# Kernel tuning notes

Hardware: AMD Instinct MI355X
Metric: run time of the kernel (lower is better)

## Reference

```python
import jax, jax.numpy as jnp
import numpy as np

V, D, H, S = 100000, 300, 300, 4096   # vocab, embed dim, biLSTM hidden (2x150), seq len
HU = H // 2                            # per-direction LSTM units
NSYN = 4


def _lstm(x, W, U, b):
    """Keras-style LSTM scan. x: [S, D] -> hidden states [S, HU]. Gate order i,f,g,o."""
    def step(carry, xt):
        h, c = carry
        z = xt @ W + h @ U + b              # [4*HU]
        i, f, g, o = jnp.split(z, 4)
        i = jax.nn.sigmoid(i)
        f = jax.nn.sigmoid(f)
        g = jnp.tanh(g)
        o = jax.nn.sigmoid(o)
        c = f * c + i * g
        h = o * jnp.tanh(c)
        return (h, c), h
    init = (jnp.zeros((HU,), x.dtype), jnp.zeros((HU,), x.dtype))
    _, hs = jax.lax.scan(step, init, x)
    return hs


def setup_inputs() -> dict:
    key = jax.random.key(0)
    ks = jax.random.split(key, 20)
    s = 0.05  # small init scale keeps exp() attention scores well-conditioned
    return {
        "sentence": jax.random.randint(ks[0], (S,), 0, V),
        "synonym_indices": jax.random.randint(ks[1], (S, NSYN), 0, V),
        "embedding_matrix": jax.random.normal(ks[2], (V, D), jnp.float32) * s,
        # forward-direction LSTM
        "W_f": jax.random.normal(ks[3], (D, 4 * HU), jnp.float32) * s,
        "U_f": jax.random.normal(ks[4], (HU, 4 * HU), jnp.float32) * s,
        "b_f": jnp.zeros((4 * HU,), jnp.float32),
        # backward-direction LSTM
        "W_b": jax.random.normal(ks[5], (D, 4 * HU), jnp.float32) * s,
        "U_b": jax.random.normal(ks[6], (HU, 4 * HU), jnp.float32) * s,
        "b_b": jnp.zeros((4 * HU,), jnp.float32),
        # primary attention dense (h1 -> h1)
        "W_p": jax.random.normal(ks[7], (H, H), jnp.float32) * s,
        "b_p": jnp.zeros((H,), jnp.float32),
        # secondary attention dense (2*h1 -> 1, tanh)
        "W_s": jax.random.normal(ks[8], (2 * H, 1), jnp.float32) * s,
        "b_s": jnp.zeros((1,), jnp.float32),
        # output heads
        "W_emo": jax.random.normal(ks[9], (2 * H, 8), jnp.float32) * s,
        "b_emo": jnp.zeros((8,), jnp.float32),
        "W_sent": jax.random.normal(ks[10], (2 * H, 1), jnp.float32) * s,
        "b_sent": jnp.zeros((1,), jnp.float32),
    }


def reference(sentence, synonym_indices, embedding_matrix,
              W_f, U_f, b_f, W_b, U_b, b_b,
              W_p, b_p, W_s, b_s, W_emo, b_emo, W_sent, b_sent):
    emb = embedding_matrix[sentence]                       # [S, D] gather
    # bidirectional LSTM (concat fwd and reversed-bwd hidden states)
    h_fwd = _lstm(emb, W_f, U_f, b_f)                      # [S, HU]
    h_bwd = _lstm(emb[::-1], W_b, U_b, b_b)[::-1]          # [S, HU]
    hidden_states = jnp.concatenate([h_fwd, h_bwd], -1)    # [S, H]
    # primary attention: per-word synonym gather + exp-scored weighted sum (vectorized)
    out = hidden_states @ W_p + b_p                        # [S, H]
    syn = embedding_matrix[synonym_indices]                # [S, NSYN, D] irregular gather
    scores = jnp.exp(jnp.einsum('sd,skd->sk', out, syn))   # [S, NSYN]
    m = jnp.einsum('sk,skd->sd', scores, syn)              # [S, D]
    h_hats = jnp.concatenate([hidden_states, m], -1)       # [S, 2H]
    # secondary attention
    coeff = jnp.exp(jnp.tanh(h_hats @ W_s + b_s))          # [S, 1]
    H_HAT = jnp.sum(coeff * h_hats, axis=0)[None, :]       # [1, 2H]
    emotion_logits = H_HAT @ W_emo + b_emo                 # [1, 8]
    sentiment_logits = H_HAT @ W_sent + b_sent             # [1, 1]
    return (emotion_logits, sentiment_logits)
```

## Files before the change

kernel.cpp:

```cpp
#include <hip/hip_runtime.h>
#include <hip/hip_bf16.h>
#include <math.h>

#define S_LEN 4096
#define D_EMB 300
#define NG    600
#define HDIM  300
#define H2    600
#define VOCAB 100000

typedef float v4f __attribute__((ext_vector_type(4)));
typedef _Float16 f16x2 __attribute__((ext_vector_type(2)));
typedef _Float16 f16x8 __attribute__((ext_vector_type(8)));

__device__ __forceinline__ float bf2f(unsigned short u) {
  union { unsigned int i; float f; } v; v.i = ((unsigned int)u) << 16; return v.f;
}
__device__ __forceinline__ unsigned short f2bf(float f) {
  union { float f; unsigned int i; } v; v.f = f;
  return (unsigned short)((v.i + 0x7FFFu + ((v.i >> 16) & 1u)) >> 16);
}

__device__ __forceinline__ void bar_lds() {
  asm volatile("s_waitcnt lgkmcnt(0)\n\ts_barrier" ::: "memory");
}

__global__ void zero_hh(float* __restrict__ HH) {
  if (threadIdx.x < 640) HH[threadIdx.x] = 0.f;
}
__global__ void zero_out_f(float* __restrict__ o, int n) {
  if ((int)threadIdx.x < n) o[threadIdx.x] = 0.f;
}

#define BM 64
#define BN 64
#define BK 16
template<bool A_BF16>
__global__ __launch_bounds__(256) void gemm_bias(
    const void* __restrict__ Av,
    const int* __restrict__ idx, int lda, int nrowsA,
    const float* __restrict__ B,
    const float* __restrict__ bias,
    unsigned short* __restrict__ C,
    int N, int K)
{
  __shared__ __align__(16) float As[BK][BM + 4];
  __shared__ __align__(16) float Bs[BK][BN + 4];
  __shared__ int rowidx[BM];

  int tid = threadIdx.x;
  int bm0 = blockIdx.y * BM, bn0 = blockIdx.x * BN;
  if (tid < BM) {
    int r = idx ? idx[bm0 + tid] : (bm0 + tid);
    r = (r < 0) ? 0 : ((r >= nrowsA) ? (nrowsA - 1) : r);
    rowidx[tid] = r;
  }
  __syncthreads();

  int tx  = tid & 15, ty = tid >> 4;
  int ar  = tid >> 2, akv = (tid & 3) << 2;
  int bkr = tid >> 4, bnv = (tid & 15) << 2;

  float acc[4][4] = {};
  for (int kk = 0; kk < K; kk += BK) {
    float a0=0.f, a1=0.f, a2=0.f, a3=0.f;
    int ka = kk + akv;
    if (ka < K) {
      if (A_BF16) {
        const unsigned short* A = (const unsigned short*)Av;
        ushort4 qa = *(const ushort4*)(A + (size_t)rowidx[ar]*lda + ka);
        a0 = bf2f(qa.x); a1 = bf2f(qa.y); a2 = bf2f(qa.z); a3 = bf2f(qa.w);
      } else {
        const float* A = (const float*)Av;
        float4 qa = *(const float4*)(A + (size_t)rowidx[ar]*lda + ka);
        a0 = qa.x; a1 = qa.y; a2 = qa.z; a3 = qa.w;
      }
    }
    float b0=0.f, b1=0.f, b2=0.f, b3=0.f;
    int kb = kk + bkr, nb = bn0 + bnv;
    if (kb < K && nb < N) {
      float4 qb = *(const float4*)(B + (size_t)kb*N + nb);
      b0 = qb.x; b1 = qb.y; b2 = qb.z; b3 = qb.w;
    }
    As[akv+0][ar] = a0; As[akv+1][ar] = a1; As[akv+2][ar] = a2; As[akv+3][ar] = a3;
    Bs[bkr][bnv+0] = b0; Bs[bkr][bnv+1] = b1; Bs[bkr][bnv+2] = b2; Bs[bkr][bnv+3] = b3;
    __syncthreads();
    #pragma unroll
    for (int k = 0; k < BK; ++k) {
      v4f av = *(const v4f*)&As[k][ty << 2];
      v4f bv = *(const v4f*)&Bs[k][tx << 2];
      #pragma unroll
      for (int i = 0; i < 4; ++i)
        #pragma unroll
        for (int j = 0; j < 4; ++j)
          acc[i][j] += av[i] * bv[j];
    }
    __syncthreads();
  }
  #pragma unroll
  for (int i = 0; i < 4; ++i) {
    int m = bm0 + (ty << 2) + i;
    #pragma unroll
    for (int j = 0; j < 4; ++j) {
      int n = bn0 + (tx << 2) + j;
      if (n < N) C[(size_t)m*N + n] = f2bf(acc[i][j] + bias[n]);
    }
  }
}

__global__ __launch_bounds__(768) void lstm_kernel(
    const unsigned short* __restrict__ pre_f, const unsigned short* __restrict__ pre_b,
    const float* __restrict__ Uf, const float* __restrict__ Ub,
    unsigned short* __restrict__ hidden )
{
  const int dir = blockIdx.x;
  const unsigned short* pre = dir ? pre_b : pre_f;
  const float* U            = dir ? Ub : Uf;
  const int tid = threadIdx.x;

  __shared__ __align__(16) unsigned short h_u16[160];
  __shared__ __align__(16) float z2[3000];
  __shared__ __align__(16) unsigned short h_hist[8][160];

  const bool faP = tid < 750;
  const bool bc  = tid < 150;
  const int c4 = tid % 150, q = tid / 150;
  const int j0 = c4 << 2;
  const int k0 = q << 5;

  f16x2 u[4][16];
  if (faP) {
    #pragma unroll
    for (int cc = 0; cc < 4; ++cc)
      #pragma unroll
      for (int p = 0; p < 16; ++p) {
        int k = k0 + (p << 1);
        float a = (k     < 150) ? U[(size_t)k    *600 + j0 + cc] : 0.f;
        float b = (k + 1 < 150) ? U[(size_t)(k+1)*600 + j0 + cc] : 0.f;
        f16x2 v; v[0] = (_Float16)a; v[1] = (_Float16)b;
        u[cc][p] = v;
      }
  }

  const int t0 = dir ? (S_LEN - 1) : 0;
  const int dt = dir ? -1 : 1;
  const ptrdiff_t pstep = (ptrdiff_t)dt * 600;

  if (tid < 160) h_u16[tid] = 0;

  float pA0=0,pA1=0,pA2=0,pA3=0, pB0=0,pB1=0,pB2=0,pB3=0;
  const unsigned short* pre2 = pre + (ptrdiff_t)t0*600 + 2*pstep;
  if (bc) {
    const unsigned short* g0 = pre + (ptrdiff_t)t0*600;
    pA0 = bf2f(g0[tid]); pA1 = bf2f(g0[tid+150]);
    pA2 = bf2f(g0[tid+300]); pA3 = bf2f(g0[tid+450]);
    const unsigned short* g1 = g0 + pstep;
    pB0 = bf2f(g1[tid]); pB1 = bf2f(g1[tid+150]);
    pB2 = bf2f(g1[tid+300]); pB3 = bf2f(g1[tid+450]);
  }
  float c = 0.f;
  __syncthreads();

  const _Float16* hf = (const _Float16*)h_u16;

  for (int s8 = 0; s8 < S_LEN/8; ++s8) {
    if (s8 && tid < 600) {
      int sub = tid / 75, w = (tid % 75) << 1;
      int sp  = (s8 << 3) - 8 + sub;
      int tp  = dir ? (S_LEN - 1 - sp) : sp;
      *(unsigned int*)(hidden + (size_t)tp*300 + dir*150 + w) =
          *(const unsigned int*)&h_hist[sub][w];
    }
    #pragma unroll
    for (int ss = 0; ss < 8; ++ss) {
      const int s = (s8 << 3) + ss;
      if (faP) {
        f16x2 hp[16];
        *(f16x8*)&hp[0]  = *(const f16x8*)&hf[k0];
        *(f16x8*)&hp[4]  = *(const f16x8*)&hf[k0 + 8];
        *(f16x8*)&hp[8]  = *(const f16x8*)&hf[k0 + 16];
        *(f16x8*)&hp[12] = *(const f16x8*)&hf[k0 + 24];
        float a0 = 0.f, a1 = 0.f, a2 = 0.f, a3 = 0.f;
        #pragma unroll
        for (int p = 0; p < 16; ++p) {
          a0 = __builtin_amdgcn_fdot2(hp[p], u[0][p], a0, false);
          a1 = __builtin_amdgcn_fdot2(hp[p], u[1][p], a1, false);
          a2 = __builtin_amdgcn_fdot2(hp[p], u[2][p], a2, false);
          a3 = __builtin_amdgcn_fdot2(hp[p], u[3][p], a3, false);
        }
        v4f zp; zp[0] = a0; zp[1] = a1; zp[2] = a2; zp[3] = a3;
        *(v4f*)&z2[q*600 + j0] = zp;
      }
      float pC0=0,pC1=0,pC2=0,pC3=0;
      if (bc && s + 2 < S_LEN) {
        pC0 = bf2f(pre2[tid]);       pC1 = bf2f(pre2[tid+150]);
        pC2 = bf2f(pre2[tid+300]);   pC3 = bf2f(pre2[tid+450]);
      }
      bar_lds();

      if (bc) {
        float zi = pA0 + ((z2[tid      ] + z2[600+tid      ]) + (z2[1200+tid      ] + z2[1800+tid      ])) + z2[2400+tid      ];
        float zf = pA1 + ((z2[tid + 150] + z2[600+tid + 150]) + (z2[1200+tid + 150] + z2[1800+tid + 150])) + z2[2400+tid + 150];
        float zg = pA2 + ((z2[tid + 300] + z2[600+tid + 300]) + (z2[1200+tid + 300] + z2[1800+tid + 300])) + z2[2400+tid + 300];
        float zo = pA3 + ((z2[tid + 450] + z2[600+tid + 450]) + (z2[1200+tid + 450] + z2[1800+tid + 450])) + z2[2400+tid + 450];
        float gi = __builtin_amdgcn_rcpf(1.f + __expf(-zi));
        float gf = __builtin_amdgcn_rcpf(1.f + __expf(-zf));
        float gg = 1.f - 2.f * __builtin_amdgcn_rcpf(__expf(2.f * zg) + 1.f);
        float go = __builtin_amdgcn_rcpf(1.f + __expf(-zo));
        c = gf * c + gi * gg;
        float th = 1.f - 2.f * __builtin_amdgcn_rcpf(__expf(2.f * c) + 1.f);
        float hv = go * th;
        ((_Float16*)h_u16)[tid] = (_Float16)hv;
        h_hist[ss][tid] = f2bf(hv);
        pA0 = pB0; pA1 = pB1; pA2 = pB2; pA3 = pB3;
        pB0 = pC0; pB1 = pC1; pB2 = pC2; pB3 = pC3;
      }
      bar_lds();
      pre2 += pstep;
    }
  }

  if (tid < 600) {
    int sub = tid / 75, w = (tid % 75) << 1;
    int sp  = S_LEN - 8 + sub;
    int tp  = dir ? (S_LEN - 1 - sp) : sp;
    *(unsigned int*)(hidden + (size_t)tp*300 + dir*150 + w) =
        *(const unsigned int*)&h_hist[sub][w];
  }
}

__global__ __launch_bounds__(128) void attn_word(
    const unsigned short* __restrict__ outp,
    const unsigned short* __restrict__ hid,
    const float* __restrict__ E,
    const int* __restrict__ syn,
    const float* __restrict__ W_s,
    const float* __restrict__ b_s,
    float* __restrict__ HH)
{
  int t = blockIdx.x, tid = threadIdx.x;
  __shared__ float s_out[300], s_hid[300], s_syn[4][300], s_m[300];
  __shared__ float s_red[8], s_sc[4], s_cf;

  int r0 = syn[t*4+0], r1 = syn[t*4+1], r2 = syn[t*4+2], r3 = syn[t*4+3];
  r0 = (r0 < 0) ? 0 : ((r0 >= VOCAB) ? VOCAB-1 : r0);
  r1 = (r1 < 0) ? 0 : ((r1 >= VOCAB) ? VOCAB-1 : r1);
  r2 = (r2 < 0) ? 0 : ((r2 >= VOCAB) ? VOCAB-1 : r2);
  r3 = (r3 < 0) ? 0 : ((r3 >= VOCAB) ? VOCAB-1 : r3);
  for (int d = tid; d < 300; d += 128) {
    s_out[d] = bf2f(outp[(size_t)t*300 + d]);
    s_hid[d] = bf2f(hid[(size_t)t*300 + d]);
    s_syn[0][d] = E[(size_t)r0*300 + d];
    s_syn[1][d] = E[(size_t)r1*300 + d];
    s_syn[2][d] = E[(size_t)r2*300 + d];
    s_syn[3][d] = E[(size_t)r3*300 + d];
  }
  __syncthreads();

  float p0=0.f, p1=0.f, p2=0.f, p3=0.f;
  for (int d = tid; d < 300; d += 128) {
    float o = s_out[d];
    p0 += o*s_syn[0][d]; p1 += o*s_syn[1][d];
    p2 += o*s_syn[2][d]; p3 += o*s_syn[3][d];
  }
  #pragma unroll
  for (int off = 32; off; off >>= 1) {
    p0 += __shfl_down(p0, off); p1 += __shfl_down(p1, off);
    p2 += __shfl_down(p2, off); p3 += __shfl_down(p3, off);
  }
  int wave = tid >> 6, lane = tid & 63;
  if (lane == 0) {
    s_red[wave*4+0] = p0; s_red[wave*4+1] = p1;
    s_red[wave*4+2] = p2; s_red[wave*4+3] = p3;
  }
  __syncthreads();
  if (tid < 4) s_sc[tid] = __expf(fminf(s_red[tid] + s_red[4 + tid], 50.f));
  __syncthreads();

  float sc0 = s_sc[0], sc1 = s_sc[1], sc2 = s_sc[2], sc3 = s_sc[3];
  float cp = 0.f;
  for (int d = tid; d < 300; d += 128) {
    float m = sc0*s_syn[0][d] + sc1*s_syn[1][d] + sc2*s_syn[2][d] + sc3*s_syn[3][d];
    s_m[d] = m;
    cp += s_hid[d]*W_s[d] + m*W_s[300 + d];
  }
  #pragma unroll
  for (int off = 32; off; off >>= 1) cp += __shfl_down(cp, off);
  if (lane == 0) s_red[wave] = cp;
  __syncthreads();
  if (tid == 0) s_cf = __expf(tanhf(s_red[0] + s_red[1] + b_s[0]));
  __syncthreads();

  float cf = s_cf;
  for (int d = tid; d < 300; d += 128) {
    atomicAdd(&HH[d],       cf * s_hid[d]);
    atomicAdd(&HH[300 + d], cf * s_m[d]);
  }
}

__global__ void heads(const float* __restrict__ HH,
                      const float* __restrict__ W_emo, const float* __restrict__ b_emo,
                      const float* __restrict__ W_sent, const float* __restrict__ b_sent,
                      float* __restrict__ out) {
  int tid = threadIdx.x;
  if (tid < 8) {
    float a = 0.f;
    for (int d = 0; d < H2; ++d) a += HH[d] * W_emo[d*8 + tid];
    out[tid] = a + b_emo[tid];
  } else if (tid == 8) {
    float a = 0.f;
    for (int d = 0; d < H2; ++d) a += HH[d] * W_sent[d];
    out[8] = a + b_sent[0];
  }
}

extern "C" void kernel_launch(void* const* d_in, const int* in_sizes, int n_in,
                              void* d_out, int out_size, void* d_ws, size_t ws_size,
                              hipStream_t stream) {
  const int*   sentence = (const int*)d_in[0];
  const int*   syn_idx  = (const int*)d_in[1];
  const float* E        = (const float*)d_in[2];
  const float* W_f      = (const float*)d_in[3];
  const float* U_f      = (const float*)d_in[4];
  const float* b_f      = (const float*)d_in[5];
  const float* W_b      = (const float*)d_in[6];
  const float* U_b      = (const float*)d_in[7];
  const float* b_b      = (const float*)d_in[8];
  const float* W_p      = (const float*)d_in[9];
  const float* b_p      = (const float*)d_in[10];
  const float* W_s      = (const float*)d_in[11];
  const float* b_s      = (const float*)d_in[12];
  const float* W_emo    = (const float*)d_in[13];
  const float* b_emo    = (const float*)d_in[14];
  const float* W_sent   = (const float*)d_in[15];
  const float* b_sent   = (const float*)d_in[16];
  float*       outv     = (float*)d_out;

  unsigned char* ws = (unsigned char*)d_ws;
  float*          HH     = (float*)ws;
  unsigned short* hidden = (unsigned short*)(ws + 2560);
  unsigned short* out_p  = (unsigned short*)(ws + 2460160);
  unsigned short* pre_f  = (unsigned short*)(ws + 4917760);
  unsigned short* pre_b  = (unsigned short*)(ws + 9832960);

  if (ws_size < 14748160u) {
    zero_out_f<<<1, 64, 0, stream>>>(outv, out_size);
    return;
  }

  zero_hh<<<1, 640, 0, stream>>>(HH);
  gemm_bias<false><<<dim3(10, 64), 256, 0, stream>>>(
      (const void*)E, sentence, D_EMB, VOCAB, W_f, b_f, pre_f, NG, D_EMB);
  gemm_bias<false><<<dim3(10, 64), 256, 0, stream>>>(
      (const void*)E, sentence, D_EMB, VOCAB, W_b, b_b, pre_b, NG, D_EMB);
  lstm_kernel<<<2, 768, 0, stream>>>(pre_f, pre_b, U_f, U_b, hidden);
  gemm_bias<true><<<dim3(5, 64), 256, 0, stream>>>(
      (const void*)hidden, nullptr, HDIM, S_LEN, W_p, b_p, out_p, HDIM, HDIM);
  attn_word<<<S_LEN, 128, 0, stream>>>(out_p, hidden, E, syn_idx, W_s, b_s, HH);
  heads<<<1, 64, 0, stream>>>(HH, W_emo, b_emo, W_sent, b_sent, outv);
}
```

Baseline: 3.621 ms.

## Use MFMA for LSTM recurrent matvec and merge fwd/bwd input GEMMs

The per-step recurrent h@U product in the LSTM kernel now runs on MFMA 16x16x32 f16 instructions across 10 wavefronts. Each wave holds a slice of U in registers as A fragments, and the hidden vector is broadcast as the B operand. Only the diagonal lanes write their results, so the five-way partial-sum reduction in LDS goes away. A separate set of 128 threads applies the gates, two units per thread for part of them. The forward and backward input-projection GEMMs are also merged into one launch using blockIdx.z. The MFMA path wastes most of its columns, because the vector is replicated across all 16 of them. In exchange, the goal is lower latency on the serial critical path of each step.

```diff
diff --git a/kernel.cpp b/kernel.cpp
--- a/kernel.cpp
+++ b/kernel.cpp
@@ -10,7 +10,6 @@
 #define VOCAB 100000
 
 typedef float v4f __attribute__((ext_vector_type(4)));
-typedef _Float16 f16x2 __attribute__((ext_vector_type(2)));
 typedef _Float16 f16x8 __attribute__((ext_vector_type(8)));
 
 __device__ __forceinline__ float bf2f(unsigned short u) {
@@ -39,11 +38,15 @@
 __global__ __launch_bounds__(256) void gemm_bias(
     const void* __restrict__ Av,
     const int* __restrict__ idx, int lda, int nrowsA,
-    const float* __restrict__ B,
-    const float* __restrict__ bias,
-    unsigned short* __restrict__ C,
+    const float* __restrict__ B0, const float* __restrict__ B1,
+    const float* __restrict__ bias0, const float* __restrict__ bias1,
+    unsigned short* __restrict__ C0, unsigned short* __restrict__ C1,
     int N, int K)
 {
+  const float* B    = blockIdx.z ? B1 : B0;
+  const float* bias = blockIdx.z ? bias1 : bias0;
+  unsigned short* C = blockIdx.z ? C1 : C0;
+
   __shared__ __align__(16) float As[BK][BM + 4];
   __shared__ __align__(16) float Bs[BK][BN + 4];
   __shared__ int rowidx[BM];
@@ -119,26 +122,32 @@
   const int tid = threadIdx.x;
 
   __shared__ __align__(16) unsigned short h_u16[160];
-  __shared__ __align__(16) float z2[3000];
+  __shared__ __align__(16) float z_lds[640];
   __shared__ __align__(16) unsigned short h_hist[8][160];
 
-  const bool faP = tid < 750;
-  const bool bc  = tid < 150;
-  const int c4 = tid % 150, q = tid / 150;
-  const int j0 = c4 << 2;
-  const int k0 = q << 5;
-
-  f16x2 u[4][16];
-  if (faP) {
-    #pragma unroll
-    for (int cc = 0; cc < 4; ++cc)
+  const int lane = tid & 63;
+  const int quad = lane >> 4;
+  const int mm   = lane & 15;
+  const int wv   = tid >> 6;
+  const bool isA  = wv < 10;
+  const bool isBC = tid >= 640;
+  const int j0 = wv << 4;
+
+  f16x8 af[4][5];
+  if (isA) {
+    #pragma unroll
+    for (int gt = 0; gt < 4; ++gt)
       #pragma unroll
-      for (int p = 0; p < 16; ++p) {
-        int k = k0 + (p << 1);
-        float a = (k     < 150) ? U[(size_t)k    *600 + j0 + cc] : 0.f;
-        float b = (k + 1 < 150) ? U[(size_t)(k+1)*600 + j0 + cc] : 0.f;
-        f16x2 v; v[0] = (_Float16)a; v[1] = (_Float16)b;
-        u[cc][p] = v;
+      for (int kc = 0; kc < 5; ++kc) {
+        f16x8 v;
+        #pragma unroll
+        for (int j = 0; j < 8; ++j) {
+          int k = kc*32 + quad*8 + j;
+          int cig = j0 + mm;
+          float x = (k < 150 && cig < 150) ? U[(size_t)k*600 + gt*150 + cig] : 0.f;
+          v[j] = (_Float16)x;
+        }
+        af[gt][kc] = v;
       }
   }
 
@@ -148,20 +157,26 @@
 
   if (tid < 160) h_u16[tid] = 0;
 
-  float pA0=0,pA1=0,pA2=0,pA3=0, pB0=0,pB1=0,pB2=0,pB3=0;
+  const int ca = tid - 640;
+  const bool hasB = isBC && (ca < 22);
+  float pA[8], pB[8];
   const unsigned short* pre2 = pre + (ptrdiff_t)t0*600 + 2*pstep;
-  if (bc) {
+  if (isBC) {
     const unsigned short* g0 = pre + (ptrdiff_t)t0*600;
-    pA0 = bf2f(g0[tid]); pA1 = bf2f(g0[tid+150]);
-    pA2 = bf2f(g0[tid+300]); pA3 = bf2f(g0[tid+450]);
     const unsigned short* g1 = g0 + pstep;
-    pB0 = bf2f(g1[tid]); pB1 = bf2f(g1[tid+150]);
-    pB2 = bf2f(g1[tid+300]); pB3 = bf2f(g1[tid+450]);
-  }
-  float c = 0.f;
+    #pragma unroll
+    for (int gt = 0; gt < 4; ++gt) {
+      pA[gt]   = bf2f(g0[gt*150 + ca]);
+      pB[gt]   = bf2f(g1[gt*150 + ca]);
+      pA[4+gt] = hasB ? bf2f(g0[gt*150 + ca + 128]) : 0.f;
+      pB[4+gt] = hasB ? bf2f(g1[gt*150 + ca + 128]) : 0.f;
+    }
+  }
+  float cA = 0.f, cB = 0.f;
   __syncthreads();
 
   const _Float16* hf = (const _Float16*)h_u16;
+  const bool wlane = (mm == quad);
 
   for (int s8 = 0; s8 < S_LEN/8; ++s8) {
     if (s8 && tid < 600) {
@@ -174,46 +189,71 @@
     #pragma unroll
     for (int ss = 0; ss < 8; ++ss) {
       const int s = (s8 << 3) + ss;
-      if (faP) {
-        f16x2 hp[16];
-        *(f16x8*)&hp[0]  = *(const f16x8*)&hf[k0];
-        *(f16x8*)&hp[4]  = *(const f16x8*)&hf[k0 + 8];
-        *(f16x8*)&hp[8]  = *(const f16x8*)&hf[k0 + 16];
-        *(f16x8*)&hp[12] = *(const f16x8*)&hf[k0 + 24];
-        float a0 = 0.f, a1 = 0.f, a2 = 0.f, a3 = 0.f;
-        #pragma unroll
-        for (int p = 0; p < 16; ++p) {
-          a0 = __builtin_amdgcn_fdot2(hp[p], u[0][p], a0, false);
-          a1 = __builtin_amdgcn_fdot2(hp[p], u[1][p], a1, false);
-          a2 = __builtin_amdgcn_fdot2(hp[p], u[2][p], a2, false);
-          a3 = __builtin_amdgcn_fdot2(hp[p], u[3][p], a3, false);
-        }
-        v4f zp; zp[0] = a0; zp[1] = a1; zp[2] = a2; zp[3] = a3;
-        *(v4f*)&z2[q*600 + j0] = zp;
-      }
-      float pC0=0,pC1=0,pC2=0,pC3=0;
-      if (bc && s + 2 < S_LEN) {
-        pC0 = bf2f(pre2[tid]);       pC1 = bf2f(pre2[tid+150]);
-        pC2 = bf2f(pre2[tid+300]);   pC3 = bf2f(pre2[tid+450]);
+      if (isA) {
+        f16x8 bfr[5];
+        #pragma unroll
+        for (int kc = 0; kc < 5; ++kc)
+          bfr[kc] = *(const f16x8*)&hf[kc*32 + quad*8];
+        v4f a0 = {0.f,0.f,0.f,0.f}, a1 = a0, a2 = a0, a3 = a0;
+        #pragma unroll
+        for (int kc = 0; kc < 5; ++kc) {
+          a0 = __builtin_amdgcn_mfma_f32_16x16x32_f16(af[0][kc], bfr[kc], a0, 0,0,0);
+          a1 = __builtin_amdgcn_mfma_f32_16x16x32_f16(af[1][kc], bfr[kc], a1, 0,0,0);
+          a2 = __builtin_amdgcn_mfma_f32_16x16x32_f16(af[2][kc], bfr[kc], a2, 0,0,0);
+          a3 = __builtin_amdgcn_mfma_f32_16x16x32_f16(af[3][kc], bfr[kc], a3, 0,0,0);
+        }
+        if (wlane) {
+          *(v4f*)&z_lds[      j0 + (quad << 2)] = a0;
+          *(v4f*)&z_lds[160 + j0 + (quad << 2)] = a1;
+          *(v4f*)&z_lds[320 + j0 + (quad << 2)] = a2;
+          *(v4f*)&z_lds[480 + j0 + (quad << 2)] = a3;
+        }
+      }
+      float pC[8];
+      if (isBC) {
+        bool ok = (s + 2 < S_LEN);
+        #pragma unroll
+        for (int gt = 0; gt < 4; ++gt) {
+          pC[gt]   = ok ? bf2f(pre2[gt*150 + ca]) : 0.f;
+          pC[4+gt] = (ok & hasB) ? bf2f(pre2[gt*150 + ca + 128]) : 0.f;
+        }
       }
       bar_lds();
 
-      if (bc) {
-        float zi = pA0 + ((z2[tid      ] + z2[600+tid      ]) + (z2[1200+tid      ] + z2[1800+tid      ])) + z2[2400+tid      ];
-        float zf = pA1 + ((z2[tid + 150] + z2[600+tid + 150]) + (z2[1200+tid + 150] + z2[1800+tid + 150])) + z2[2400+tid + 150];
-        float zg = pA2 + ((z2[tid + 300] + z2[600+tid + 300]) + (z2[1200+tid + 300] + z2[1800+tid + 300])) + z2[2400+tid + 300];
-        float zo = pA3 + ((z2[tid + 450] + z2[600+tid + 450]) + (z2[1200+tid + 450] + z2[1800+tid + 450])) + z2[2400+tid + 450];
-        float gi = __builtin_amdgcn_rcpf(1.f + __expf(-zi));
-        float gf = __builtin_amdgcn_rcpf(1.f + __expf(-zf));
-        float gg = 1.f - 2.f * __builtin_amdgcn_rcpf(__expf(2.f * zg) + 1.f);
-        float go = __builtin_amdgcn_rcpf(1.f + __expf(-zo));
-        c = gf * c + gi * gg;
-        float th = 1.f - 2.f * __builtin_amdgcn_rcpf(__expf(2.f * c) + 1.f);
-        float hv = go * th;
-        ((_Float16*)h_u16)[tid] = (_Float16)hv;
-        h_hist[ss][tid] = f2bf(hv);
-        pA0 = pB0; pA1 = pB1; pA2 = pB2; pA3 = pB3;
-        pB0 = pC0; pB1 = pC1; pB2 = pC2; pB3 = pC3;
+      if (isBC) {
+        {
+          float zi = z_lds[      ca] + pA[0];
+          float zf = z_lds[160 + ca] + pA[1];
+          float zg = z_lds[320 + ca] + pA[2];
+          float zo = z_lds[480 + ca] + pA[3];
+          float gi = __builtin_amdgcn_rcpf(1.f + __expf(-zi));
+          float gf = __builtin_amdgcn_rcpf(1.f + __expf(-zf));
+          float gg = 1.f - 2.f * __builtin_amdgcn_rcpf(__expf(2.f * zg) + 1.f);
+          float go = __builtin_amdgcn_rcpf(1.f + __expf(-zo));
+          cA = gf * cA + gi * gg;
+          float th = 1.f - 2.f * __builtin_amdgcn_rcpf(__expf(2.f * cA) + 1.f);
+          float hv = go * th;
+          ((_Float16*)h_u16)[ca] = (_Float16)hv;
+          h_hist[ss][ca] = f2bf(hv);
+        }
+        if (hasB) {
+          int cb = ca + 128;
+          float zi = z_lds[      cb] + pA[4];
+          float zf = z_lds[160 + cb] + pA[5];
+          float zg = z_lds[320 + cb] + pA[6];
+          float zo = z_lds[480 + cb] + pA[7];
+          float gi = __builtin_amdgcn_rcpf(1.f + __expf(-zi));
+          float gf = __builtin_amdgcn_rcpf(1.f + __expf(-zf));
+          float gg = 1.f - 2.f * __builtin_amdgcn_rcpf(__expf(2.f * zg) + 1.f);
+          float go = __builtin_amdgcn_rcpf(1.f + __expf(-zo));
+          cB = gf * cB + gi * gg;
+          float th = 1.f - 2.f * __builtin_amdgcn_rcpf(__expf(2.f * cB) + 1.f);
+          float hv = go * th;
+          ((_Float16*)h_u16)[cb] = (_Float16)hv;
+          h_hist[ss][cb] = f2bf(hv);
+        }
+        #pragma unroll
+        for (int i = 0; i < 8; ++i) { pA[i] = pB[i]; pB[i] = pC[i]; }
       }
       bar_lds();
       pre2 += pstep;
@@ -349,13 +389,11 @@
   }
 
   zero_hh<<<1, 640, 0, stream>>>(HH);
-  gemm_bias<false><<<dim3(10, 64), 256, 0, stream>>>(
-      (const void*)E, sentence, D_EMB, VOCAB, W_f, b_f, pre_f, NG, D_EMB);
-  gemm_bias<false><<<dim3(10, 64), 256, 0, stream>>>(
-      (const void*)E, sentence, D_EMB, VOCAB, W_b, b_b, pre_b, NG, D_EMB);
+  gemm_bias<false><<<dim3(10, 64, 2), 256, 0, stream>>>(
+      (const void*)E, sentence, D_EMB, VOCAB, W_f, W_b, b_f, b_b, pre_f, pre_b, NG, D_EMB);
   lstm_kernel<<<2, 768, 0, stream>>>(pre_f, pre_b, U_f, U_b, hidden);
-  gemm_bias<true><<<dim3(5, 64), 256, 0, stream>>>(
-      (const void*)hidden, nullptr, HDIM, S_LEN, W_p, b_p, out_p, HDIM, HDIM);
+  gemm_bias<true><<<dim3(5, 64, 1), 256, 0, stream>>>(
+      (const void*)hidden, nullptr, HDIM, S_LEN, W_p, W_p, b_p, b_p, out_p, out_p, HDIM, HDIM);
   attn_word<<<S_LEN, 128, 0, stream>>>(out_p, hidden, E, syn_idx, W_s, b_s, HH);
   heads<<<1, 64, 0, stream>>>(HH, W_emo, b_emo, W_sent, b_sent, outv);
 }
```

Result: slower. 10.71 ms (+195.7%).
